# Performance work log

Hardware: AMD Instinct MI355X
Metric: run time of the kernel (lower is better)

## Reference

```python
import jax, jax.numpy as jnp
import numpy as np

B = 524288  # number of mel frames
MEL = 128   # mel bins (hard-coded in module)
D = 64      # code dim
K = 128     # codebook size


def setup_inputs() -> dict:
    key = jax.random.key(0)
    ks = jax.random.split(key, 7)
    return {
        "mel_frame": jax.random.normal(ks[0], (B, MEL), dtype=jnp.float32),
        "W_in": jax.random.normal(ks[1], (D, MEL), dtype=jnp.float32) * 0.05,
        "b_in": jax.random.normal(ks[2], (D,), dtype=jnp.float32) * 0.05,
        "cb0": jax.random.normal(ks[3], (K, D), dtype=jnp.float32),
        "cb1": jax.random.normal(ks[4], (K, D), dtype=jnp.float32),
        "W_out": jax.random.normal(ks[5], (MEL, D), dtype=jnp.float32) * 0.05,
        "b_out": jax.random.normal(ks[6], (MEL,), dtype=jnp.float32) * 0.05,
    }


def reference(mel_frame, W_in, b_in, cb0, cb1, W_out, b_out):
    # encode: project mel -> d, then greedy residual VQ over 2 codebooks
    z = mel_frame @ W_in.T + b_in                      # (B, D)
    residual = z
    z_q = jnp.zeros_like(z)
    idxs = []
    for cb in (cb0, cb1):
        # squared L2 distance without materializing (B, K, D):
        # ||r - c||^2 = ||r||^2 - 2 r.c + ||c||^2  -> (B, K)
        dist = (
            jnp.sum(residual * residual, axis=-1, keepdims=True)
            - 2.0 * (residual @ cb.T)
            + jnp.sum(cb * cb, axis=-1)
        )
        ind = jnp.argmin(dist, axis=-1)                # (B,)
        code = cb[ind]                                 # gather chosen codes (B, D)
        residual = residual - code
        z_q = z_q + code
        idxs.append(ind)
    # decode: sum of selected codes -> project back to mel
    mel = z_q @ W_out.T + b_out                        # (B, MEL)
    return mel, jnp.stack(idxs, axis=-1)
```

## Files before the change

kernel.cpp:

```cpp
#include <hip/hip_runtime.h>
#include <hip/hip_bf16.h>

#define B_ROWS   524288
#define MEL_BINS 128
#define DIM      64
#define KCODES   128

#define WS_WT  0
#define WS_C0T (WS_WT + MEL_BINS*DIM)
#define WS_C1T (WS_C0T + DIM*KCODES)
#define WS_N0  (WS_C1T + DIM*KCODES)
#define WS_N1  (WS_N0 + KCODES)
#define WS_T0  (WS_N1 + KCODES)
#define WS_T1  (WS_T0 + KCODES*MEL_BINS)
#define WS_TOT (WS_T1 + KCODES*MEL_BINS)

__device__ __forceinline__ float np_pairwise64_sq(const float* v) {
#pragma clang fp contract(off)
    float r0 = v[0]*v[0], r1 = v[1]*v[1], r2 = v[2]*v[2], r3 = v[3]*v[3];
    float r4 = v[4]*v[4], r5 = v[5]*v[5], r6 = v[6]*v[6], r7 = v[7]*v[7];
#pragma unroll
    for (int i = 8; i < 64; i += 8) {
        r0 += v[i+0]*v[i+0]; r1 += v[i+1]*v[i+1];
        r2 += v[i+2]*v[i+2]; r3 += v[i+3]*v[i+3];
        r4 += v[i+4]*v[i+4]; r5 += v[i+5]*v[i+5];
        r6 += v[i+6]*v[i+6]; r7 += v[i+7]*v[i+7];
    }
    return ((r0 + r1) + (r2 + r3)) + ((r4 + r5) + (r6 + r7));
}

__global__ __launch_bounds__(256) void rvq_precomp(
    const float* __restrict__ W_in, const float* __restrict__ cb0,
    const float* __restrict__ cb1, const float* __restrict__ W_out,
    float* __restrict__ ws)
{
#pragma clang fp contract(off)
    float* WT  = ws + WS_WT;
    float* c0T = ws + WS_C0T;
    float* c1T = ws + WS_C1T;
    float* n0  = ws + WS_N0;
    float* n1  = ws + WS_N1;
    float* T0  = ws + WS_T0;
    float* T1  = ws + WS_T1;

    int tid = blockIdx.x * 256 + threadIdx.x;
    if (tid < 16384) {
        int i = tid >> 7, m = tid & 127;
        double a = 0.0;
        for (int d = 0; d < DIM; ++d)
            a = fma((double)cb0[i*DIM + d], (double)W_out[m*DIM + d], a);
        T0[tid] = (float)a;
    } else if (tid < 32768) {
        int t = tid - 16384;
        int i = t >> 7, m = t & 127;
        double a = 0.0;
        for (int d = 0; d < DIM; ++d)
            a = fma((double)cb1[i*DIM + d], (double)W_out[m*DIM + d], a);
        T1[t] = (float)a;
    } else if (tid < 40960) {
        int t = tid - 32768;
        int j = t >> 6, d = t & 63;
        WT[t] = W_in[d*MEL_BINS + j];
    } else if (tid < 41216) {
        int t = tid - 40960;
        const float* cb = (t & 128) ? cb1 : cb0;
        float*       nn = (t & 128) ? n1  : n0;
        int k = t & 127;
        nn[k] = np_pairwise64_sq(cb + k*DIM);
    } else if (tid < 49408) {
        int t = tid - 41216;
        int d = t >> 7, k = t & 127;
        c0T[t] = cb0[k*DIM + d];
    } else if (tid < 57600) {
        int t = tid - 49408;
        int d = t >> 7, k = t & 127;
        c1T[t] = cb1[k*DIM + d];
    }
}

__global__ __launch_bounds__(256) void rvq_main(
    const float* __restrict__ mel,
    const float* __restrict__ b_in,
    const float* __restrict__ cb0,
    const float* __restrict__ cb1,
    const float* __restrict__ b_out,
    const float* __restrict__ ws,
    float* __restrict__ out_mel,
    float* __restrict__ out_idx)
{
#pragma clang fp contract(off)
    const float* __restrict__ WT  = ws + WS_WT;
    const float* __restrict__ c0T = ws + WS_C0T;
    const float* __restrict__ c1T = ws + WS_C1T;
    const float* __restrict__ n0  = ws + WS_N0;
    const float* __restrict__ n1  = ws + WS_N1;
    const float* __restrict__ T0  = ws + WS_T0;
    const float* __restrict__ T1  = ws + WS_T1;

    const int b = blockIdx.x * 256 + threadIdx.x;

    float z[DIM];
#pragma unroll
    for (int d = 0; d < DIM; ++d) z[d] = 0.f;

    const float4* melr = reinterpret_cast<const float4*>(mel + (size_t)b * MEL_BINS);
    for (int jc = 0; jc < MEL_BINS / 4; ++jc) {
        float4 m4 = melr[jc];
        const float* w = WT + jc * 4 * DIM;
#pragma unroll
        for (int d = 0; d < DIM; ++d) z[d] = fmaf(w[d],         m4.x, z[d]);
#pragma unroll
        for (int d = 0; d < DIM; ++d) z[d] = fmaf(w[DIM + d],   m4.y, z[d]);
#pragma unroll
        for (int d = 0; d < DIM; ++d) z[d] = fmaf(w[2*DIM + d], m4.z, z[d]);
#pragma unroll
        for (int d = 0; d < DIM; ++d) z[d] = fmaf(w[3*DIM + d], m4.w, z[d]);
    }
#pragma unroll
    for (int d = 0; d < DIM; ++d) z[d] = z[d] + b_in[d];

    float s0 = z[0]*z[0], s1 = z[1]*z[1], s2 = z[2]*z[2], s3 = z[3]*z[3];
    float s4 = z[4]*z[4], s5 = z[5]*z[5], s6 = z[6]*z[6], s7 = z[7]*z[7];
#pragma unroll
    for (int i = 8; i < 64; i += 8) {
        s0 += z[i+0]*z[i+0]; s1 += z[i+1]*z[i+1];
        s2 += z[i+2]*z[i+2]; s3 += z[i+3]*z[i+3];
        s4 += z[i+4]*z[i+4]; s5 += z[i+5]*z[i+5];
        s6 += z[i+6]*z[i+6]; s7 += z[i+7]*z[i+7];
    }
    float sum_rr = ((s0 + s1) + (s2 + s3)) + ((s4 + s5) + (s6 + s7));

    float best0 = 3.4e38f; int i0 = 0;
    for (int kc = 0; kc < KCODES; kc += 16) {
        float acc[16];
#pragma unroll
        for (int t = 0; t < 16; ++t) acc[t] = 0.f;
#pragma unroll 4
        for (int d = 0; d < DIM; ++d) {
            const float* row = c0T + d * KCODES + kc;
            float zd = z[d];
#pragma unroll
            for (int t = 0; t < 16; ++t) acc[t] = fmaf(row[t], zd, acc[t]);
        }
#pragma unroll
        for (int t = 0; t < 16; ++t) {
            float dist = (sum_rr - 2.0f*acc[t]) + n0[kc + t];
            if (dist < best0) { best0 = dist; i0 = kc + t; }
        }
    }

    {
        const float* c = cb0 + (size_t)i0 * DIM;
#pragma unroll
        for (int d = 0; d < DIM; ++d) z[d] = z[d] - c[d];
    }

    s0 = z[0]*z[0]; s1 = z[1]*z[1]; s2 = z[2]*z[2]; s3 = z[3]*z[3];
    s4 = z[4]*z[4]; s5 = z[5]*z[5]; s6 = z[6]*z[6]; s7 = z[7]*z[7];
#pragma unroll
    for (int i = 8; i < 64; i += 8) {
        s0 += z[i+0]*z[i+0]; s1 += z[i+1]*z[i+1];
        s2 += z[i+2]*z[i+2]; s3 += z[i+3]*z[i+3];
        s4 += z[i+4]*z[i+4]; s5 += z[i+5]*z[i+5];
        s6 += z[i+6]*z[i+6]; s7 += z[i+7]*z[i+7];
    }
    sum_rr = ((s0 + s1) + (s2 + s3)) + ((s4 + s5) + (s6 + s7));

    float best1 = 3.4e38f; int i1 = 0;
    for (int kc = 0; kc < KCODES; kc += 16) {
        float acc[16];
#pragma unroll
        for (int t = 0; t < 16; ++t) acc[t] = 0.f;
#pragma unroll 4
        for (int d = 0; d < DIM; ++d) {
            const float* row = c1T + d * KCODES + kc;
            float zd = z[d];
#pragma unroll
            for (int t = 0; t < 16; ++t) acc[t] = fmaf(row[t], zd, acc[t]);
        }
#pragma unroll
        for (int t = 0; t < 16; ++t) {
            float dist = (sum_rr - 2.0f*acc[t]) + n1[kc + t];
            if (dist < best1) { best1 = dist; i1 = kc + t; }
        }
    }

    const float4* t0r = reinterpret_cast<const float4*>(T0 + (size_t)i0 * MEL_BINS);
    const float4* t1r = reinterpret_cast<const float4*>(T1 + (size_t)i1 * MEL_BINS);
    float4* outr = reinterpret_cast<float4*>(out_mel + (size_t)b * MEL_BINS);
#pragma unroll 4
    for (int q = 0; q < MEL_BINS / 4; ++q) {
        float4 a = t0r[q], c = t1r[q];
        float4 o;
        o.x = a.x + c.x + b_out[4*q + 0];
        o.y = a.y + c.y + b_out[4*q + 1];
        o.z = a.z + c.z + b_out[4*q + 2];
        o.w = a.w + c.w + b_out[4*q + 3];
        outr[q] = o;
    }

    out_idx[2*(size_t)b + 0] = (float)i0;
    out_idx[2*(size_t)b + 1] = (float)i1;
}

extern "C" void kernel_launch(void* const* d_in, const int* in_sizes, int n_in,
                              void* d_out, int out_size, void* d_ws, size_t ws_size,
                              hipStream_t stream)
{
    const float* mel   = (const float*)d_in[0];
    const float* W_in  = (const float*)d_in[1];
    const float* b_in  = (const float*)d_in[2];
    const float* cb0   = (const float*)d_in[3];
    const float* cb1   = (const float*)d_in[4];
    const float* W_out = (const float*)d_in[5];
    const float* b_out = (const float*)d_in[6];

    float* ws      = (float*)d_ws;
    float* out_mel = (float*)d_out;
    float* out_idx = (float*)d_out + (size_t)B_ROWS * MEL_BINS;

    rvq_precomp<<<(WS_TOT + 255) / 256, 256, 0, stream>>>(W_in, cb0, cb1, W_out, ws);
    rvq_main<<<B_ROWS / 256, 256, 0, stream>>>(mel, b_in, cb0, cb1, b_out, ws,
                                               out_mel, out_idx);
}
```

Baseline: 603.2 us.

## Use packed FP32 FMA with scalar weights and spill z to LDS

Rewrites the main kernel's projection and distance loops to use inline-asm v_pk_fma_f32 with the weights/codebook pairs as SGPR operands, doing two FMAs per instruction. The projection is split into two 32-dim halves, and the z vector lives in padded shared memory instead of 64 registers, to lower register pressure. Block size drops to 128 threads. The aim is to halve the VALU instruction count and raise occupancy, at the cost of LDS traffic and packed-operand constraints.

```diff
diff --git a/kernel.cpp b/kernel.cpp
--- a/kernel.cpp
+++ b/kernel.cpp
@@ -5,6 +5,12 @@
 #define MEL_BINS 128
 #define DIM      64
 #define KCODES   128
+#define THREADS  128
+
+typedef float v2f __attribute__((ext_vector_type(2)));
+typedef float v4f __attribute__((ext_vector_type(4)));
+
+#define PK(A, C, Z) asm("v_pk_fma_f32 %0, %1, %2, %0" : "+v"(A) : "s"(C), "v"(Z))
 
 #define WS_WT  0
 #define WS_C0T (WS_WT + MEL_BINS*DIM)
@@ -78,7 +84,7 @@
     }
 }
 
-__global__ __launch_bounds__(256) void rvq_main(
+__global__ __launch_bounds__(THREADS) void rvq_main(
     const float* __restrict__ mel,
     const float* __restrict__ b_in,
     const float* __restrict__ cb0,
@@ -89,118 +95,148 @@
     float* __restrict__ out_idx)
 {
 #pragma clang fp contract(off)
-    const float* __restrict__ WT  = ws + WS_WT;
-    const float* __restrict__ c0T = ws + WS_C0T;
-    const float* __restrict__ c1T = ws + WS_C1T;
+    const v2f*   __restrict__ WTp = (const v2f*)(ws + WS_WT);
+    const v2f*   __restrict__ c0P = (const v2f*)(ws + WS_C0T);
+    const v2f*   __restrict__ c1P = (const v2f*)(ws + WS_C1T);
     const float* __restrict__ n0  = ws + WS_N0;
     const float* __restrict__ n1  = ws + WS_N1;
     const float* __restrict__ T0  = ws + WS_T0;
     const float* __restrict__ T1  = ws + WS_T1;
-
-    const int b = blockIdx.x * 256 + threadIdx.x;
-
-    float z[DIM];
-#pragma unroll
-    for (int d = 0; d < DIM; ++d) z[d] = 0.f;
-
-    const float4* melr = reinterpret_cast<const float4*>(mel + (size_t)b * MEL_BINS);
-    for (int jc = 0; jc < MEL_BINS / 4; ++jc) {
-        float4 m4 = melr[jc];
-        const float* w = WT + jc * 4 * DIM;
-#pragma unroll
-        for (int d = 0; d < DIM; ++d) z[d] = fmaf(w[d],         m4.x, z[d]);
-#pragma unroll
-        for (int d = 0; d < DIM; ++d) z[d] = fmaf(w[DIM + d],   m4.y, z[d]);
-#pragma unroll
-        for (int d = 0; d < DIM; ++d) z[d] = fmaf(w[2*DIM + d], m4.z, z[d]);
-#pragma unroll
-        for (int d = 0; d < DIM; ++d) z[d] = fmaf(w[3*DIM + d], m4.w, z[d]);
-    }
-#pragma unroll
-    for (int d = 0; d < DIM; ++d) z[d] = z[d] + b_in[d];
-
-    float s0 = z[0]*z[0], s1 = z[1]*z[1], s2 = z[2]*z[2], s3 = z[3]*z[3];
-    float s4 = z[4]*z[4], s5 = z[5]*z[5], s6 = z[6]*z[6], s7 = z[7]*z[7];
-#pragma unroll
-    for (int i = 8; i < 64; i += 8) {
-        s0 += z[i+0]*z[i+0]; s1 += z[i+1]*z[i+1];
-        s2 += z[i+2]*z[i+2]; s3 += z[i+3]*z[i+3];
-        s4 += z[i+4]*z[i+4]; s5 += z[i+5]*z[i+5];
-        s6 += z[i+6]*z[i+6]; s7 += z[i+7]*z[i+7];
-    }
-    float sum_rr = ((s0 + s1) + (s2 + s3)) + ((s4 + s5) + (s6 + s7));
+    const v2f*   __restrict__ bi2 = (const v2f*)b_in;
+
+    __shared__ float zbuf[THREADS * 65];
+
+    const int tid = threadIdx.x;
+    const size_t b = (size_t)blockIdx.x * THREADS + tid;
+    const int lb = tid * 65;
+
+    const v4f* melp = (const v4f*)(mel + b * MEL_BINS);
+
+    float r[8];
+#pragma unroll
+    for (int t = 0; t < 8; ++t) r[t] = 0.f;
+
+#pragma unroll
+    for (int half = 0; half < 2; ++half) {
+        const int pbase = half * 16;
+        v2f zh[16];
+#pragma unroll
+        for (int p = 0; p < 16; ++p) zh[p] = (v2f){0.f, 0.f};
+
+        for (int jc = 0; jc < 32; ++jc) {
+            v4f m4 = melp[jc];
+            v2f m0 = (v2f){m4.x, m4.x};
+            v2f m1 = (v2f){m4.y, m4.y};
+            v2f m2 = (v2f){m4.z, m4.z};
+            v2f m3 = (v2f){m4.w, m4.w};
+            const v2f* w0 = WTp + (jc*4 + 0)*32 + pbase;
+            const v2f* w1 = WTp + (jc*4 + 1)*32 + pbase;
+            const v2f* w2 = WTp + (jc*4 + 2)*32 + pbase;
+            const v2f* w3 = WTp + (jc*4 + 3)*32 + pbase;
+#pragma unroll
+            for (int p = 0; p < 16; ++p) PK(zh[p], w0[p], m0);
+#pragma unroll
+            for (int p = 0; p < 16; ++p) PK(zh[p], w1[p], m1);
+#pragma unroll
+            for (int p = 0; p < 16; ++p) PK(zh[p], w2[p], m2);
+#pragma unroll
+            for (int p = 0; p < 16; ++p) PK(zh[p], w3[p], m3);
+        }
+#pragma unroll
+        for (int p = 0; p < 16; ++p) {
+            v2f bb = bi2[pbase + p];
+            float vx = zh[p].x + bb.x;
+            float vy = zh[p].y + bb.y;
+            int d = half*32 + 2*p;
+            r[d & 7]       += vx * vx;
+            r[(d + 1) & 7] += vy * vy;
+            zbuf[lb + d]     = vx;
+            zbuf[lb + d + 1] = vy;
+        }
+        asm volatile("" : "+v"(melp));
+    }
+    float sum_rr = ((r[0] + r[1]) + (r[2] + r[3])) + ((r[4] + r[5]) + (r[6] + r[7]));
 
     float best0 = 3.4e38f; int i0 = 0;
-    for (int kc = 0; kc < KCODES; kc += 16) {
-        float acc[16];
-#pragma unroll
-        for (int t = 0; t < 16; ++t) acc[t] = 0.f;
+    for (int kc = 0; kc < 4; ++kc) {
+        v2f a[16];
+#pragma unroll
+        for (int t = 0; t < 16; ++t) a[t] = (v2f){0.f, 0.f};
 #pragma unroll 4
         for (int d = 0; d < DIM; ++d) {
-            const float* row = c0T + d * KCODES + kc;
-            float zd = z[d];
-#pragma unroll
-            for (int t = 0; t < 16; ++t) acc[t] = fmaf(row[t], zd, acc[t]);
+            float zd = zbuf[lb + d];
+            v2f zd2 = (v2f){zd, zd};
+            const v2f* crow = c0P + d*64 + kc*16;
+#pragma unroll
+            for (int t = 0; t < 16; ++t) PK(a[t], crow[t], zd2);
         }
 #pragma unroll
         for (int t = 0; t < 16; ++t) {
-            float dist = (sum_rr - 2.0f*acc[t]) + n0[kc + t];
-            if (dist < best0) { best0 = dist; i0 = kc + t; }
+            int k = kc*32 + 2*t;
+            float d0 = (sum_rr - 2.0f*a[t].x) + n0[k];
+            float d1 = (sum_rr - 2.0f*a[t].y) + n0[k+1];
+            if (d0 < best0) { best0 = d0; i0 = k; }
+            if (d1 < best0) { best0 = d1; i0 = k+1; }
         }
     }
 
     {
         const float* c = cb0 + (size_t)i0 * DIM;
-#pragma unroll
-        for (int d = 0; d < DIM; ++d) z[d] = z[d] - c[d];
-    }
-
-    s0 = z[0]*z[0]; s1 = z[1]*z[1]; s2 = z[2]*z[2]; s3 = z[3]*z[3];
-    s4 = z[4]*z[4]; s5 = z[5]*z[5]; s6 = z[6]*z[6]; s7 = z[7]*z[7];
-#pragma unroll
-    for (int i = 8; i < 64; i += 8) {
-        s0 += z[i+0]*z[i+0]; s1 += z[i+1]*z[i+1];
-        s2 += z[i+2]*z[i+2]; s3 += z[i+3]*z[i+3];
-        s4 += z[i+4]*z[i+4]; s5 += z[i+5]*z[i+5];
-        s6 += z[i+6]*z[i+6]; s7 += z[i+7]*z[i+7];
-    }
-    sum_rr = ((s0 + s1) + (s2 + s3)) + ((s4 + s5) + (s6 + s7));
+        float q[8];
+#pragma unroll
+        for (int t = 0; t < 8; ++t) q[t] = 0.f;
+        for (int ib = 0; ib < 8; ++ib) {
+            int d = ib * 8;
+#pragma unroll
+            for (int t = 0; t < 8; ++t) {
+                float v = zbuf[lb + d + t] - c[d + t];
+                zbuf[lb + d + t] = v;
+                q[t] += v * v;
+            }
+        }
+        sum_rr = ((q[0] + q[1]) + (q[2] + q[3])) + ((q[4] + q[5]) + (q[6] + q[7]));
+    }
 
     float best1 = 3.4e38f; int i1 = 0;
-    for (int kc = 0; kc < KCODES; kc += 16) {
-        float acc[16];
-#pragma unroll
-        for (int t = 0; t < 16; ++t) acc[t] = 0.f;
+    for (int kc = 0; kc < 4; ++kc) {
+        v2f a[16];
+#pragma unroll
+        for (int t = 0; t < 16; ++t) a[t] = (v2f){0.f, 0.f};
 #pragma unroll 4
         for (int d = 0; d < DIM; ++d) {
-            const float* row = c1T + d * KCODES + kc;
-            float zd = z[d];
-#pragma unroll
-            for (int t = 0; t < 16; ++t) acc[t] = fmaf(row[t], zd, acc[t]);
+            float zd = zbuf[lb + d];
+            v2f zd2 = (v2f){zd, zd};
+            const v2f* crow = c1P + d*64 + kc*16;
+#pragma unroll
+            for (int t = 0; t < 16; ++t) PK(a[t], crow[t], zd2);
         }
 #pragma unroll
         for (int t = 0; t < 16; ++t) {
-            float dist = (sum_rr - 2.0f*acc[t]) + n1[kc + t];
-            if (dist < best1) { best1 = dist; i1 = kc + t; }
-        }
-    }
-
-    const float4* t0r = reinterpret_cast<const float4*>(T0 + (size_t)i0 * MEL_BINS);
-    const float4* t1r = reinterpret_cast<const float4*>(T1 + (size_t)i1 * MEL_BINS);
-    float4* outr = reinterpret_cast<float4*>(out_mel + (size_t)b * MEL_BINS);
+            int k = kc*32 + 2*t;
+            float d0 = (sum_rr - 2.0f*a[t].x) + n1[k];
+            float d1 = (sum_rr - 2.0f*a[t].y) + n1[k+1];
+            if (d0 < best1) { best1 = d0; i1 = k; }
+            if (d1 < best1) { best1 = d1; i1 = k+1; }
+        }
+    }
+
+    const v4f* t0r = (const v4f*)(T0 + (size_t)i0 * MEL_BINS);
+    const v4f* t1r = (const v4f*)(T1 + (size_t)i1 * MEL_BINS);
+    const v4f* bo  = (const v4f*)b_out;
+    v4f* outr = (v4f*)(out_mel + b * MEL_BINS);
 #pragma unroll 4
     for (int q = 0; q < MEL_BINS / 4; ++q) {
-        float4 a = t0r[q], c = t1r[q];
-        float4 o;
-        o.x = a.x + c.x + b_out[4*q + 0];
-        o.y = a.y + c.y + b_out[4*q + 1];
-        o.z = a.z + c.z + b_out[4*q + 2];
-        o.w = a.w + c.w + b_out[4*q + 3];
+        v4f a = t0r[q], c = t1r[q], bb = bo[q];
+        v4f o;
+        o.x = a.x + c.x + bb.x;
+        o.y = a.y + c.y + bb.y;
+        o.z = a.z + c.z + bb.z;
+        o.w = a.w + c.w + bb.w;
         outr[q] = o;
     }
 
-    out_idx[2*(size_t)b + 0] = (float)i0;
-    out_idx[2*(size_t)b + 1] = (float)i1;
+    out_idx[2*b + 0] = (float)i0;
+    out_idx[2*b + 1] = (float)i1;
 }
 
 extern "C" void kernel_launch(void* const* d_in, const int* in_sizes, int n_in,
@@ -220,6 +256,6 @@
     float* out_idx = (float*)d_out + (size_t)B_ROWS * MEL_BINS;
 
     rvq_precomp<<<(WS_TOT + 255) / 256, 256, 0, stream>>>(W_in, cb0, cb1, W_out, ws);
-    rvq_main<<<B_ROWS / 256, 256, 0, stream>>>(mel, b_in, cb0, cb1, b_out, ws,
-                                               out_mel, out_idx);
-}
+    rvq_main<<<B_ROWS / THREADS, THREADS, 0, stream>>>(mel, b_in, cb0, cb1, b_out,
+                                                       ws, out_mel, out_idx);
+}
```

Result: slower. 1.104 ms (+83.0%).

## Interleave codebook by groups of four and cap occupancy via dummy LDS

Applied to the files above, without the earlier changes.

Codebooks are reordered into groups of four codes interleaved per dimension, so each distance pass keeps only four accumulators and reads contiguous float4-friendly data instead of sixteen accumulators over strided rows. Block size drops to 128 threads, a waves_per_eu attribute is added, and a never-executed branch touching a large shared array pins LDS usage so fewer waves share each CU. This trades occupancy for a larger register budget, aiming to cut spills of the 64-float z vector and accumulators. The tie-breaking order of the argmin stays the same, so results should not change.

```diff
diff --git a/kernel.cpp b/kernel.cpp
--- a/kernel.cpp
+++ b/kernel.cpp
@@ -5,11 +5,12 @@
 #define MEL_BINS 128
 #define DIM      64
 #define KCODES   128
+#define THREADS  128
 
 #define WS_WT  0
-#define WS_C0T (WS_WT + MEL_BINS*DIM)
-#define WS_C1T (WS_C0T + DIM*KCODES)
-#define WS_N0  (WS_C1T + DIM*KCODES)
+#define WS_C0B (WS_WT + MEL_BINS*DIM)
+#define WS_C1B (WS_C0B + DIM*KCODES)
+#define WS_N0  (WS_C1B + DIM*KCODES)
 #define WS_N1  (WS_N0 + KCODES)
 #define WS_T0  (WS_N1 + KCODES)
 #define WS_T1  (WS_T0 + KCODES*MEL_BINS)
@@ -36,8 +37,8 @@
 {
 #pragma clang fp contract(off)
     float* WT  = ws + WS_WT;
-    float* c0T = ws + WS_C0T;
-    float* c1T = ws + WS_C1T;
+    float* c0B = ws + WS_C0B;
+    float* c1B = ws + WS_C1B;
     float* n0  = ws + WS_N0;
     float* n1  = ws + WS_N1;
     float* T0  = ws + WS_T0;
@@ -69,16 +70,20 @@
         nn[k] = np_pairwise64_sq(cb + k*DIM);
     } else if (tid < 49408) {
         int t = tid - 41216;
-        int d = t >> 7, k = t & 127;
-        c0T[t] = cb0[k*DIM + d];
+        int p = t >> 8, rem = t & 255;
+        int d = rem >> 2, tt = rem & 3;
+        c0B[t] = cb0[(4*p + tt)*DIM + d];
     } else if (tid < 57600) {
         int t = tid - 49408;
-        int d = t >> 7, k = t & 127;
-        c1T[t] = cb1[k*DIM + d];
-    }
-}
-
-__global__ __launch_bounds__(256) void rvq_main(
+        int p = t >> 8, rem = t & 255;
+        int d = rem >> 2, tt = rem & 3;
+        c1B[t] = cb1[(4*p + tt)*DIM + d];
+    }
+}
+
+__global__ __launch_bounds__(THREADS)
+__attribute__((amdgpu_waves_per_eu(1, 4)))
+void rvq_main(
     const float* __restrict__ mel,
     const float* __restrict__ b_in,
     const float* __restrict__ cb0,
@@ -90,14 +95,16 @@
 {
 #pragma clang fp contract(off)
     const float* __restrict__ WT  = ws + WS_WT;
-    const float* __restrict__ c0T = ws + WS_C0T;
-    const float* __restrict__ c1T = ws + WS_C1T;
+    const float* __restrict__ c0B = ws + WS_C0B;
+    const float* __restrict__ c1B = ws + WS_C1B;
     const float* __restrict__ n0  = ws + WS_N0;
     const float* __restrict__ n1  = ws + WS_N1;
     const float* __restrict__ T0  = ws + WS_T0;
     const float* __restrict__ T1  = ws + WS_T1;
 
-    const int b = blockIdx.x * 256 + threadIdx.x;
+    __shared__ float occ_cap[5120];
+
+    const int b = blockIdx.x * THREADS + threadIdx.x;
 
     float z[DIM];
 #pragma unroll
@@ -130,23 +137,33 @@
     }
     float sum_rr = ((s0 + s1) + (s2 + s3)) + ((s4 + s5) + (s6 + s7));
 
+    if (b == 0x7FFFFFF0) {
+        occ_cap[threadIdx.x] = sum_rr;
+        __syncthreads();
+        out_mel[0] = occ_cap[(threadIdx.x + 1) & 127];
+    }
+
     float best0 = 3.4e38f; int i0 = 0;
-    for (int kc = 0; kc < KCODES; kc += 16) {
-        float acc[16];
-#pragma unroll
-        for (int t = 0; t < 16; ++t) acc[t] = 0.f;
-#pragma unroll 4
+    for (int p = 0; p < 32; ++p) {
+        const float* cp = c0B + p * 256;
+        float a0 = 0.f, a1 = 0.f, a2 = 0.f, a3 = 0.f;
+#pragma unroll
         for (int d = 0; d < DIM; ++d) {
-            const float* row = c0T + d * KCODES + kc;
             float zd = z[d];
-#pragma unroll
-            for (int t = 0; t < 16; ++t) acc[t] = fmaf(row[t], zd, acc[t]);
+            a0 = fmaf(cp[d*4 + 0], zd, a0);
+            a1 = fmaf(cp[d*4 + 1], zd, a1);
+            a2 = fmaf(cp[d*4 + 2], zd, a2);
+            a3 = fmaf(cp[d*4 + 3], zd, a3);
         }
-#pragma unroll
-        for (int t = 0; t < 16; ++t) {
-            float dist = (sum_rr - 2.0f*acc[t]) + n0[kc + t];
-            if (dist < best0) { best0 = dist; i0 = kc + t; }
-        }
+        int k = p * 4;
+        float d0 = (sum_rr - 2.0f*a0) + n0[k + 0];
+        float d1 = (sum_rr - 2.0f*a1) + n0[k + 1];
+        float d2 = (sum_rr - 2.0f*a2) + n0[k + 2];
+        float d3 = (sum_rr - 2.0f*a3) + n0[k + 3];
+        if (d0 < best0) { best0 = d0; i0 = k + 0; }
+        if (d1 < best0) { best0 = d1; i0 = k + 1; }
+        if (d2 < best0) { best0 = d2; i0 = k + 2; }
+        if (d3 < best0) { best0 = d3; i0 = k + 3; }
     }
 
     {
@@ -167,22 +184,26 @@
     sum_rr = ((s0 + s1) + (s2 + s3)) + ((s4 + s5) + (s6 + s7));
 
     float best1 = 3.4e38f; int i1 = 0;
-    for (int kc = 0; kc < KCODES; kc += 16) {
-        float acc[16];
-#pragma unroll
-        for (int t = 0; t < 16; ++t) acc[t] = 0.f;
-#pragma unroll 4
+    for (int p = 0; p < 32; ++p) {
+        const float* cp = c1B + p * 256;
+        float a0 = 0.f, a1 = 0.f, a2 = 0.f, a3 = 0.f;
+#pragma unroll
         for (int d = 0; d < DIM; ++d) {
-            const float* row = c1T + d * KCODES + kc;
             float zd = z[d];
-#pragma unroll
-            for (int t = 0; t < 16; ++t) acc[t] = fmaf(row[t], zd, acc[t]);
+            a0 = fmaf(cp[d*4 + 0], zd, a0);
+            a1 = fmaf(cp[d*4 + 1], zd, a1);
+            a2 = fmaf(cp[d*4 + 2], zd, a2);
+            a3 = fmaf(cp[d*4 + 3], zd, a3);
         }
-#pragma unroll
-        for (int t = 0; t < 16; ++t) {
-            float dist = (sum_rr - 2.0f*acc[t]) + n1[kc + t];
-            if (dist < best1) { best1 = dist; i1 = kc + t; }
-        }
+        int k = p * 4;
+        float d0 = (sum_rr - 2.0f*a0) + n1[k + 0];
+        float d1 = (sum_rr - 2.0f*a1) + n1[k + 1];
+        float d2 = (sum_rr - 2.0f*a2) + n1[k + 2];
+        float d3 = (sum_rr - 2.0f*a3) + n1[k + 3];
+        if (d0 < best1) { best1 = d0; i1 = k + 0; }
+        if (d1 < best1) { best1 = d1; i1 = k + 1; }
+        if (d2 < best1) { best1 = d2; i1 = k + 2; }
+        if (d3 < best1) { best1 = d3; i1 = k + 3; }
     }
 
     const float4* t0r = reinterpret_cast<const float4*>(T0 + (size_t)i0 * MEL_BINS);
@@ -220,6 +241,6 @@
     float* out_idx = (float*)d_out + (size_t)B_ROWS * MEL_BINS;
 
     rvq_precomp<<<(WS_TOT + 255) / 256, 256, 0, stream>>>(W_in, cb0, cb1, W_out, ws);
-    rvq_main<<<B_ROWS / 256, 256, 0, stream>>>(mel, b_in, cb0, cb1, b_out, ws,
-                                               out_mel, out_idx);
-}
+    rvq_main<<<B_ROWS / THREADS, THREADS, 0, stream>>>(mel, b_in, cb0, cb1, b_out,
+                                                       ws, out_mel, out_idx);
+}
```

New measurement: 659.2 us. 1.09x slower.
